# Performance work log

Measured on AMD Instinct MI355X. Metric: run time of the kernel, lower is better.

Reference implementation:

```python
import jax, jax.numpy as jnp
import numpy as np

LN2 = jnp.log(jnp.float32(2.0))
ALPHA = 0.5          # alpha_pool = [0.5]
A_BITS = 8           # activation bit width (BIT_TYPE_A)
W_BITS = 8           # weight bit width (BIT_TYPE_W)
EPS = 1e-8


def round_ln(x):
    # 'round' branch: floor(log2(x)) then pick nearer power of two
    y = jnp.floor(jnp.log(x) / LN2)
    up = (x - 2.0 ** y) > (2.0 ** (y + 1.0) - x)
    return y + up.astype(x.dtype)


def fq_act_asym(x, bits=A_BITS):
    # per-tensor asymmetric uniform fake-quant (QAct min-max observer)
    qmax = 2 ** bits - 1
    xmin = jnp.minimum(x.min(), 0.0)
    xmax = jnp.maximum(x.max(), 0.0)
    scale = jnp.maximum((xmax - xmin) / qmax, EPS)
    zp = jnp.round(-xmin / scale)
    q = jnp.clip(jnp.round(x / scale) + zp, 0, qmax)
    return (q - zp) * scale


def fq_act_sym(x, bits=A_BITS):
    # per-tensor symmetric fake-quant (qact1 with asymmetric=False)
    qmax = 2 ** (bits - 1) - 1
    scale = jnp.maximum(jnp.abs(x).max() / qmax, EPS)
    q = jnp.clip(jnp.round(x / scale), -qmax - 1, qmax)
    return q * scale


def fq_weight(w, bits=W_BITS):
    # per-output-channel symmetric weight fake-quant (QLinear)
    qmax = 2 ** (bits - 1) - 1
    scale = jnp.maximum(jnp.abs(w).max(axis=1, keepdims=True) / qmax, EPS)
    q = jnp.clip(jnp.round(w / scale), -qmax - 1, qmax)
    return q * scale


def setup_inputs() -> dict:
    key = jax.random.key(0)
    ks = jax.random.split(key, 5)
    B, N, C, H = 64, 197, 768, 3072
    x = jax.random.normal(ks[0], (B, N, C), dtype=jnp.float32)
    w1 = jax.random.normal(ks[1], (H, C), dtype=jnp.float32) * 0.02
    b1 = jax.random.normal(ks[2], (H,), dtype=jnp.float32) * 0.02
    w2 = jax.random.normal(ks[3], (C, H), dtype=jnp.float32) * 0.02
    b2 = jax.random.normal(ks[4], (C,), dtype=jnp.float32) * 0.02
    return {"x": x, "w1": w1, "b1": b1, "w2": w2, "b2": b2}


def reference(x, w1, b1, w2, b2):
    # ---- smoothquant power-of-two channel scale (fc1 input channels) ----
    global_max_x = jnp.abs(x).max(axis=(0, 1))      # [C]
    max_weight = jnp.abs(w1).max(axis=0)            # [C]
    cs = global_max_x ** ALPHA / max_weight ** (1.0 - ALPHA)
    cs = 2.0 ** round_ln(cs)                        # snap to power of two
    x_smoothed = x / cs[None, None, :]
    w1_smoothed = w1 * cs[None, :]
    # ---- qact0 -> fc1 (8-bit fake-quant GEMM) ----
    xq = fq_act_asym(x_smoothed)
    h = jnp.einsum('bnc,hc->bnh', xq, fq_weight(w1_smoothed)) + b1
    # ---- act (exact GELU, nn.GELU default) -> qact1 (symmetric) ----
    h = jax.nn.gelu(h, approximate=False)
    hq = fq_act_sym(h)
    # ---- fc2 -> qact2 ----
    out = jnp.einsum('bnh,ch->bnc', hq, fq_weight(w2)) + b2
    out = fq_act_asym(out)
    return out
```

## Files before the change

### kernel.cpp

```cpp
#include <hip/hip_runtime.h>
#include <cstdint>
#include <cstddef>

typedef int v4i __attribute__((ext_vector_type(4)));

#define DI static __device__ __forceinline__

DI unsigned fmap(float f){ unsigned b=__float_as_uint(f); return (b&0x80000000u)? ~b : (b|0x80000000u); }
DI float funmap(unsigned u){ return (u&0x80000000u)? __uint_as_float(u&0x7fffffffu) : __uint_as_float(~u); }
DI float gelu_f(float x){ return 0.5f*x*(1.0f+erff(x*0.70710678118654752440f)); }

constexpr int Mtok = 12608;
constexpr int Cdim = 768;
constexpr int Hdim = 3072;
constexpr int MP   = 12672;

__global__ void k_init(unsigned* scal, unsigned* xminU, unsigned* xmaxU, unsigned* wmaxU){
    int t = blockIdx.x*256 + threadIdx.x;
    if (t < Cdim){
        xminU[t] = fmap(__builtin_inff());
        xmaxU[t] = fmap(-__builtin_inff());
        wmaxU[t] = fmap(0.0f);
    }
    if (t == 0){
        scal[0] = fmap(0.0f);
        scal[1] = fmap(__builtin_inff());
        scal[2] = fmap(-__builtin_inff());
    }
}

__global__ void k_colstats_x(const float* __restrict__ x, unsigned* xminU, unsigned* xmaxU){
    int t = threadIdx.x;
    float mn0= __builtin_inff(), mn1= __builtin_inff(), mn2= __builtin_inff();
    float mx0=-__builtin_inff(), mx1=-__builtin_inff(), mx2=-__builtin_inff();
    for (int r = blockIdx.x; r < Mtok; r += gridDim.x){
        const float* row = x + (size_t)r*Cdim;
        float v0=row[t], v1=row[t+256], v2=row[t+512];
        mn0=fminf(mn0,v0); mx0=fmaxf(mx0,v0);
        mn1=fminf(mn1,v1); mx1=fmaxf(mx1,v1);
        mn2=fminf(mn2,v2); mx2=fmaxf(mx2,v2);
    }
    atomicMin(&xminU[t      ], fmap(mn0)); atomicMax(&xmaxU[t      ], fmap(mx0));
    atomicMin(&xminU[t+256  ], fmap(mn1)); atomicMax(&xmaxU[t+256  ], fmap(mx1));
    atomicMin(&xminU[t+512  ], fmap(mn2)); atomicMax(&xmaxU[t+512  ], fmap(mx2));
}

__global__ void k_colmax_w1(const float* __restrict__ w1, unsigned* wmaxU){
    int t = threadIdx.x;
    float m0=0.f, m1=0.f, m2=0.f;
    for (int r = blockIdx.x; r < Hdim; r += gridDim.x){
        const float* row = w1 + (size_t)r*Cdim;
        m0=fmaxf(m0,fabsf(row[t]));
        m1=fmaxf(m1,fabsf(row[t+256]));
        m2=fmaxf(m2,fabsf(row[t+512]));
    }
    atomicMax(&wmaxU[t      ], fmap(m0));
    atomicMax(&wmaxU[t+256  ], fmap(m1));
    atomicMax(&wmaxU[t+512  ], fmap(m2));
}

__global__ void k_scale0(const unsigned* xminU, const unsigned* xmaxU, const unsigned* wmaxU,
                         float* cs, unsigned* scal){
    __shared__ float smn[256], smx[256];
    int t = threadIdx.x;
    float lmn =  __builtin_inff(), lmx = -__builtin_inff();
    #pragma unroll
    for (int j = 0; j < 3; ++j){
        int c = t + j*256;
        float xn = funmap(xminU[c]), xm = funmap(xmaxU[c]), wm = funmap(wmaxU[c]);
        float g  = fmaxf(fabsf(xn), fabsf(xm));
        float csr = powf(g, 0.5f) / powf(wm, 0.5f);
        float y = floorf(logf(csr) / 0.6931471805599453f);
        float p = exp2f(y);
        float c2 = exp2f(y + (((csr - p) > (2.0f*p - csr)) ? 1.0f : 0.0f));
        cs[c] = c2;
        lmn = fminf(lmn, xn / c2);
        lmx = fmaxf(lmx, xm / c2);
    }
    smn[t]=lmn; smx[t]=lmx; __syncthreads();
    for (int s=128; s; s>>=1){
        if (t < s){ smn[t]=fminf(smn[t],smn[t+s]); smx[t]=fmaxf(smx[t],smx[t+s]); }
        __syncthreads();
    }
    if (t == 0){
        float xmin_t = fminf(smn[0], 0.0f);
        float xmax_t = fmaxf(smx[0], 0.0f);
        float sc = fmaxf((xmax_t - xmin_t)/255.0f, 1e-8f);
        float zp = rintf(-xmin_t/sc);
        float* fs = (float*)scal;
        fs[8] = sc; fs[9] = zp;
    }
}

__global__ void k_quant_w1(const float* __restrict__ w1, const float* __restrict__ cs,
                           const unsigned* scal, int8_t* __restrict__ qw1,
                           float* sa1, int* icorr1){
    __shared__ float sm[256];
    __shared__ int   si[256];
    int h = blockIdx.x, t = threadIdx.x;
    const float* wr = w1 + (size_t)h*Cdim;
    float v0 = wr[t]*cs[t], v1 = wr[t+256]*cs[t+256], v2 = wr[t+512]*cs[t+512];
    float am = fmaxf(fabsf(v0), fmaxf(fabsf(v1), fabsf(v2)));
    sm[t]=am; __syncthreads();
    for (int s=128; s; s>>=1){ if (t<s) sm[t]=fmaxf(sm[t],sm[t+s]); __syncthreads(); }
    float scale = fmaxf(sm[0]/127.0f, 1e-8f);
    float q0 = fminf(fmaxf(rintf(v0/scale), -128.0f), 127.0f);
    float q1 = fminf(fmaxf(rintf(v1/scale), -128.0f), 127.0f);
    float q2 = fminf(fmaxf(rintf(v2/scale), -128.0f), 127.0f);
    qw1[(size_t)h*Cdim + t      ] = (int8_t)q0;
    qw1[(size_t)h*Cdim + t + 256] = (int8_t)q1;
    qw1[(size_t)h*Cdim + t + 512] = (int8_t)q2;
    si[t] = (int)q0 + (int)q1 + (int)q2; __syncthreads();
    for (int s=128; s; s>>=1){ if (t<s) si[t]+=si[t+s]; __syncthreads(); }
    if (t == 0){
        const float* fs = (const float*)scal;
        sa1[h]    = fs[8]*scale;
        icorr1[h] = (128 - (int)fs[9]) * si[0];
    }
}

__global__ void k_quant_w2(const float* __restrict__ w2, int8_t* __restrict__ qw2, float* sa2){
    __shared__ float sm[256];
    int c = blockIdx.x, t = threadIdx.x;
    const float* wr = w2 + (size_t)c*Hdim;
    float v[12]; float am = 0.f;
    #pragma unroll
    for (int j=0;j<12;++j){ v[j]=wr[t + j*256]; am=fmaxf(am,fabsf(v[j])); }
    sm[t]=am; __syncthreads();
    for (int s=128; s; s>>=1){ if (t<s) sm[t]=fmaxf(sm[t],sm[t+s]); __syncthreads(); }
    float scale = fmaxf(sm[0]/127.0f, 1e-8f);
    #pragma unroll
    for (int j=0;j<12;++j){
        float q = fminf(fmaxf(rintf(v[j]/scale), -128.0f), 127.0f);
        qw2[(size_t)c*Hdim + t + j*256] = (int8_t)q;
    }
    if (t == 0) sa2[c] = scale;
}

__global__ void k_quant_x(const float* __restrict__ x, const float* __restrict__ cs,
                          const unsigned* scal, int8_t* __restrict__ qxs){
    int idx = blockIdx.x*256 + threadIdx.x;
    const int total = Mtok*(Cdim/4);
    if (idx >= total) return;
    const float* fs = (const float*)scal;
    float sc = fs[8], zp = fs[9];
    float4 v = ((const float4*)x)[idx];
    int cb = (idx % (Cdim/4))*4;
    float q0 = fminf(fmaxf(rintf((v.x/cs[cb+0])/sc)+zp, 0.f), 255.f);
    float q1 = fminf(fmaxf(rintf((v.y/cs[cb+1])/sc)+zp, 0.f), 255.f);
    float q2 = fminf(fmaxf(rintf((v.z/cs[cb+2])/sc)+zp, 0.f), 255.f);
    float q3 = fminf(fmaxf(rintf((v.w/cs[cb+3])/sc)+zp, 0.f), 255.f);
    uint32_t pack =  (uint32_t)(uint8_t)((int)q0-128)
                  | ((uint32_t)(uint8_t)((int)q1-128) << 8)
                  | ((uint32_t)(uint8_t)((int)q2-128) << 16)
                  | ((uint32_t)(uint8_t)((int)q3-128) << 24);
    ((uint32_t*)qxs)[idx] = pack;
}

#define GLL(src,dst) __builtin_amdgcn_global_load_lds( \
    (const __attribute__((address_space(1))) unsigned*)(src), \
    (__attribute__((address_space(3))) unsigned*)(dst), 16, 0, 0)

#define WAITVM8 asm volatile("s_waitcnt vmcnt(8)" ::: "memory")
#define WAITVM4 asm volatile("s_waitcnt vmcnt(4)" ::: "memory")
#define WAITVM0 asm volatile("s_waitcnt vmcnt(0)" ::: "memory")

template<int KSTEPS, int MODE, int NY>
__global__ __launch_bounds__(256)
void k_gemm(const int8_t* __restrict__ A, const int8_t* __restrict__ Bw, int N,
            const float* __restrict__ sa, const int* __restrict__ icorr,
            const float* __restrict__ bias, const unsigned* __restrict__ scal,
            int8_t* __restrict__ qout, float* __restrict__ fout, _Float16* __restrict__ hout,
            unsigned* __restrict__ r0, unsigned* __restrict__ r1)
{
    constexpr int K = KSTEPS*64;
    __shared__ __align__(16) int8_t LDSB[49152];
    __shared__ float sred[8];
    int t = threadIdx.x, lane = t & 63, wid = t >> 6;
    int wr = wid >> 1, wc = wid & 1;

    int nwg = gridDim.x;
    int q8 = nwg >> 3, r8 = nwg & 7;
    int xcd = blockIdx.x & 7, li = blockIdx.x >> 3;
    int swz = (xcd < r8 ? xcd*(q8+1) : r8*(q8+1) + (xcd - r8)*q8) + li;
    int bx = swz / NY, by = swz % NY;
    size_t brow = (size_t)bx * 128;
    int bcol = by * 128;

    int srow = t >> 2;
    int schunk = (t & 3) ^ ((srow >> 1) & 3);
    const int8_t* ga0 = A  + (brow + srow)*(size_t)K + schunk*16;
    const int8_t* gb0 = Bw + (size_t)(bcol + srow)*K + schunk*16;

    int rsw  = ((lane >> 4) ^ ((lane >> 1) & 3)) << 4;
    int aoff = ((wr*64 + (lane & 15)) << 6) + rsw;
    int boff = 8192 + ((wc*64 + (lane & 15)) << 6) + rsw;

    float sav[4], bbv[4]; int icv[4]; float sh = 0.f;
    #pragma unroll
    for (int n=0;n<4;++n){
        int col = bcol + wc*64 + n*16 + (lane & 15);
        sav[n] = sa[col];
        bbv[n] = bias[col];
        icv[n] = (MODE == 2) ? 0 : icorr[col];
    }
    if (MODE == 1 || MODE == 2) sh = fmaxf(funmap(*scal)/127.0f, 1e-8f);
    asm volatile("" ::: "memory");

#define STAGE(cur, ks) do{ \
    const int8_t* pa_ = ga0 + (ks)*64; \
    const int8_t* pb_ = gb0 + (ks)*64; \
    int8_t* ld_ = LDSB + (cur)*16384 + t*16; \
    GLL(pa_,                ld_); \
    GLL(pa_ + (size_t)64*K, ld_ + 4096); \
    GLL(pb_,                ld_ + 8192); \
    GLL(pb_ + (size_t)64*K, ld_ + 12288); \
}while(0)

    v4i acc[4][4] = {};
    STAGE(0,0); STAGE(1,1); STAGE(2,2);

#define ITER(cur, ks, WAITM, RESTAGE) do{ \
    WAITM;                                    \
    __builtin_amdgcn_s_barrier();             \
    const int8_t* bp_ = LDSB + (cur)*16384; \
    v4i a_[4], b_[4]; \
    _Pragma("unroll") \
    for (int m_=0;m_<4;++m_) a_[m_] = *(const v4i*)(bp_ + aoff + (m_<<10)); \
    _Pragma("unroll") \
    for (int n_=0;n_<4;++n_) b_[n_] = *(const v4i*)(bp_ + boff + (n_<<10)); \
    asm volatile("s_waitcnt lgkmcnt(0)" ::: "memory"); \
    __builtin_amdgcn_sched_barrier(0); \
    __builtin_amdgcn_s_barrier();             \
    if (RESTAGE) STAGE(cur, (ks)+3); \
    __builtin_amdgcn_s_setprio(1); \
    _Pragma("unroll") \
    for (int m_=0;m_<4;++m_) \
        _Pragma("unroll") \
        for (int n_=0;n_<4;++n_) \
            acc[m_][n_] = __builtin_amdgcn_mfma_i32_16x16x64_i8(a_[m_], b_[n_], acc[m_][n_], 0, 0, 0); \
    __builtin_amdgcn_s_setprio(0); \
}while(0)

    constexpr int MAING = (KSTEPS - 3)/3;
    for (int kg = 0; kg < MAING; ++kg){
        int ks = kg*3;
        ITER(0, ks,   WAITVM8, true);
        ITER(1, ks+1, WAITVM8, true);
        ITER(2, ks+2, WAITVM8, true);
    }
    ITER(0, KSTEPS-3, WAITVM8, false);
    ITER(1, KSTEPS-2, WAITVM4, false);
    ITER(2, KSTEPS-1, WAITVM0, false);
#undef ITER
#undef STAGE

    int rl = (lane >> 4) * 4;
    if (MODE == 0){
        float amax = 0.f;
        #pragma unroll
        for (int n=0;n<4;++n){
            #pragma unroll
            for (int m=0;m<4;++m){
                size_t row = brow + wr*64 + m*16 + rl;
                #pragma unroll
                for (int r=0;r<4;++r){
                    if (row + r < (size_t)Mtok){
                        float g = gelu_f(sav[n]*(float)(acc[m][n][r] + icv[n]) + bbv[n]);
                        amax = fmaxf(amax, fabsf(g));
                    }
                }
            }
        }
        #pragma unroll
        for (int off=32; off; off>>=1) amax = fmaxf(amax, __shfl_down(amax, off));
        if (lane == 0) sred[wid] = amax;
        __syncthreads();
        if (t == 0) atomicMax(r0, fmap(fmaxf(fmaxf(sred[0],sred[1]), fmaxf(sred[2],sred[3]))));
    } else if (MODE == 1){
        #pragma unroll
        for (int n=0;n<4;++n){
            int col = bcol + wc*64 + n*16 + (lane & 15);
            #pragma unroll
            for (int m=0;m<4;++m){
                size_t row = brow + wr*64 + m*16 + rl;
                #pragma unroll
                for (int r=0;r<4;++r){
                    if (row + r < (size_t)Mtok){
                        float g = gelu_f(sav[n]*(float)(acc[m][n][r] + icv[n]) + bbv[n]);
                        float qv = fminf(fmaxf(rintf(g/sh), -128.0f), 127.0f);
                        qout[(row + r)*(size_t)N + col] = (int8_t)qv;
                    }
                }
            }
        }
    } else if (MODE == 3){
        float amax = 0.f;
        _Float16* hb = hout + ((size_t)(bx*NY + by))*16384 + (size_t)t*64;
        #pragma unroll
        for (int n=0;n<4;++n){
            #pragma unroll
            for (int m=0;m<4;++m){
                size_t row = brow + wr*64 + m*16 + rl;
                union { _Float16 h4[4]; uint2 u2; } pk;
                #pragma unroll
                for (int r=0;r<4;++r){
                    float g = gelu_f(sav[n]*(float)(acc[m][n][r] + icv[n]) + bbv[n]);
                    if (row + r < (size_t)Mtok) amax = fmaxf(amax, fabsf(g));
                    pk.h4[r] = (_Float16)g;
                }
                ((uint2*)hb)[n*4 + m] = pk.u2;
            }
        }
        #pragma unroll
        for (int off=32; off; off>>=1) amax = fmaxf(amax, __shfl_down(amax, off));
        if (lane == 0) sred[wid] = amax;
        __syncthreads();
        if (t == 0) atomicMax(r0, fmap(fmaxf(fmaxf(sred[0],sred[1]), fmaxf(sred[2],sred[3]))));
    } else {
        float lmin =  __builtin_inff(), lmax = -__builtin_inff();
        float* ob = fout + ((size_t)(bx*NY + by))*16384 + (size_t)t*64;
        #pragma unroll
        for (int n=0;n<4;++n){
            float s = sh * sav[n];
            #pragma unroll
            for (int m=0;m<4;++m){
                size_t row = brow + wr*64 + m*16 + rl;
                float4 o4;
                #pragma unroll
                for (int r=0;r<4;++r){
                    float o = s*(float)acc[m][n][r] + bbv[n];
                    if (row + r < (size_t)Mtok){ lmin = fminf(lmin, o); lmax = fmaxf(lmax, o); }
                    ((float*)&o4)[r] = o;
                }
                ((float4*)ob)[n*4 + m] = o4;
            }
        }
        #pragma unroll
        for (int off=32; off; off>>=1){
            lmin = fminf(lmin, __shfl_down(lmin, off));
            lmax = fmaxf(lmax, __shfl_down(lmax, off));
        }
        if (lane == 0){ sred[wid] = lmin; sred[4+wid] = lmax; }
        __syncthreads();
        if (t == 0){
            atomicMin(r0, fmap(fminf(fminf(sred[0],sred[1]), fminf(sred[2],sred[3]))));
            atomicMax(r1, fmap(fmaxf(fmaxf(sred[4],sred[5]), fmaxf(sred[6],sred[7]))));
        }
    }
}

__global__ void k_requant(const _Float16* __restrict__ h, const unsigned* __restrict__ scal,
                          int8_t* __restrict__ qh){
    int idx = blockIdx.x*256 + threadIdx.x;
    const int total = Mtok*(Hdim/8);
    if (idx >= total) return;
    float sh = fmaxf(funmap(scal[0])/127.0f, 1e-8f);
    int R  = idx / 384;
    int cb = (idx - R*384) * 8;
    int bx = R >> 7, r0 = R & 127;
    int by = cb >> 7;
    int wr = r0 >> 6, m = (r0 >> 4) & 3, lhi = (r0 >> 2) & 3, r = r0 & 3;
    int wc = (cb >> 6) & 1, n = (cb >> 4) & 3, li0 = cb & 15;
    int tb = (wr*2 + wc)*64 + lhi*16 + li0;
    const _Float16* p = h + ((size_t)(bx*24 + by))*16384 + (size_t)tb*64 + ((n*4 + m)*4 + r);
    uint32_t lo = 0, hi = 0;
    #pragma unroll
    for (int j=0;j<4;++j){
        float q = fminf(fmaxf(rintf((float)p[j*64]/sh), -128.0f), 127.0f);
        lo |= ((uint32_t)(uint8_t)(int)q) << (8*j);
    }
    #pragma unroll
    for (int j=0;j<4;++j){
        float q = fminf(fmaxf(rintf((float)p[(4+j)*64]/sh), -128.0f), 127.0f);
        hi |= ((uint32_t)(uint8_t)(int)q) << (8*j);
    }
    uint2 pk; pk.x = lo; pk.y = hi;
    ((uint2*)qh)[idx] = pk;
}

__global__ void k_final(const float* __restrict__ outpre, const unsigned* __restrict__ scal,
                        float* __restrict__ out){
    int idx = blockIdx.x*256 + threadIdx.x;
    const int total = Mtok*(Cdim/4);
    if (idx >= total) return;
    float omin = fminf(funmap(scal[1]), 0.0f);
    float omax = fmaxf(funmap(scal[2]), 0.0f);
    float sc = fmaxf((omax - omin)/255.0f, 1e-8f);
    float zp = rintf(-omin/sc);
    int R  = idx / 192;
    int cb = (idx - R*192) * 4;
    int bx = R >> 7, r0 = R & 127;
    int by = cb >> 7;
    int wr = r0 >> 6, m = (r0 >> 4) & 3, lhi = (r0 >> 2) & 3, r = r0 & 3;
    int wc = (cb >> 6) & 1, n = (cb >> 4) & 3, li0 = cb & 15;
    int tb = (wr*2 + wc)*64 + lhi*16 + li0;
    const float* p = outpre + ((size_t)(bx*6 + by))*16384 + (size_t)tb*64 + ((n*4 + m)*4 + r);
    float4 v;
    v.x = p[0]; v.y = p[64]; v.z = p[128]; v.w = p[192];
    v.x = (fminf(fmaxf(rintf(v.x/sc)+zp, 0.f), 255.f) - zp)*sc;
    v.y = (fminf(fmaxf(rintf(v.y/sc)+zp, 0.f), 255.f) - zp)*sc;
    v.z = (fminf(fmaxf(rintf(v.z/sc)+zp, 0.f), 255.f) - zp)*sc;
    v.w = (fminf(fmaxf(rintf(v.w/sc)+zp, 0.f), 255.f) - zp)*sc;
    ((float4*)out)[idx] = v;
}

extern "C" void kernel_launch(void* const* d_in, const int* in_sizes, int n_in,
                              void* d_out, int out_size, void* d_ws, size_t ws_size,
                              hipStream_t stream)
{
    if (n_in < 5) return;
    const float* x  = (const float*)d_in[0];
    const float* w1 = (const float*)d_in[1];
    const float* b1 = (const float*)d_in[2];
    const float* w2 = (const float*)d_in[3];
    const float* b2 = (const float*)d_in[4];
    float* out = (float*)d_out;

    uint8_t* w = (uint8_t*)d_ws;
    size_t off = 0;
    unsigned* scal  = (unsigned*)(w + off); off += 256;
    unsigned* xminU = (unsigned*)(w + off); off += 3072;
    unsigned* xmaxU = (unsigned*)(w + off); off += 3072;
    unsigned* wmaxU = (unsigned*)(w + off); off += 3072;
    float*    cs    = (float*)   (w + off); off += 3072;
    float*    sa1   = (float*)   (w + off); off += 12288;
    int*      icorr1= (int*)     (w + off); off += 12288;
    float*    sa2   = (float*)   (w + off); off += 3072;
    off = (off + 255) & ~(size_t)255;
    int8_t*   qw1   = (int8_t*)  (w + off); off += (size_t)Hdim*Cdim;
    int8_t*   qw2   = (int8_t*)  (w + off); off += (size_t)Cdim*Hdim;
    int8_t*   qxs   = (int8_t*)  (w + off); off += (size_t)MP*Cdim;
    int8_t*   qh    = (int8_t*)  (w + off); off += (size_t)MP*Hdim;
    size_t off_big = off;
    float*    outpre= (float*)   (w + off_big);
    _Float16* hbuf  = (_Float16*)(w + off_big);
    size_t need_3g  = off_big + (size_t)99*6*16384*4;
    size_t need_h16 = off_big + (size_t)99*24*16384*2;
    if (ws_size < need_3g) return;
    bool use_h16 = (ws_size >= need_h16);

    k_init<<<3, 256, 0, stream>>>(scal, xminU, xmaxU, wmaxU);
    k_colstats_x<<<512, 256, 0, stream>>>(x, xminU, xmaxU);
    k_colmax_w1<<<512, 256, 0, stream>>>(w1, wmaxU);
    k_scale0<<<1, 256, 0, stream>>>(xminU, xmaxU, wmaxU, cs, scal);
    k_quant_w1<<<Hdim, 256, 0, stream>>>(w1, cs, scal, qw1, sa1, icorr1);
    k_quant_w2<<<Cdim, 256, 0, stream>>>(w2, qw2, sa2);
    k_quant_x<<<(Mtok*(Cdim/4) + 255)/256, 256, 0, stream>>>(x, cs, scal, qxs);

    if (use_h16){
        k_gemm<12,3,24><<<2376, 256, 0, stream>>>(qxs, qw1, Hdim, sa1, icorr1, b1, scal,
                                                  nullptr, nullptr, hbuf, &scal[0], nullptr);
        k_requant<<<(Mtok*(Hdim/8) + 255)/256, 256, 0, stream>>>(hbuf, scal, qh);
    } else {
        k_gemm<12,0,24><<<2376, 256, 0, stream>>>(qxs, qw1, Hdim, sa1, icorr1, b1, scal,
                                                  nullptr, nullptr, nullptr, &scal[0], nullptr);
        k_gemm<12,1,24><<<2376, 256, 0, stream>>>(qxs, qw1, Hdim, sa1, icorr1, b1, scal,
                                                  qh, nullptr, nullptr, nullptr, nullptr);
    }
    k_gemm<48,2,6><<<594, 256, 0, stream>>>(qh, qw2, Cdim, sa2, nullptr, b2, scal,
                                            nullptr, outpre, nullptr, &scal[1], &scal[2]);

    k_final<<<(Mtok*(Cdim/4) + 255)/256, 256, 0, stream>>>(outpre, scal, out);
}
```

Baseline: 387.5 us.

## Load GEMM B operand directly to registers and coalesce staged epilogue writes

```diff
diff --git a/kernel.cpp b/kernel.cpp
--- a/kernel.cpp
+++ b/kernel.cpp
@@ -161,10 +161,6 @@
     (const __attribute__((address_space(1))) unsigned*)(src), \
     (__attribute__((address_space(3))) unsigned*)(dst), 16, 0, 0)
 
-#define WAITVM8 asm volatile("s_waitcnt vmcnt(8)" ::: "memory")
-#define WAITVM4 asm volatile("s_waitcnt vmcnt(4)" ::: "memory")
-#define WAITVM0 asm volatile("s_waitcnt vmcnt(0)" ::: "memory")
-
 template<int KSTEPS, int MODE, int NY>
 __global__ __launch_bounds__(256)
 void k_gemm(const int8_t* __restrict__ A, const int8_t* __restrict__ Bw, int N,
@@ -174,7 +170,7 @@
             unsigned* __restrict__ r0, unsigned* __restrict__ r1)
 {
     constexpr int K = KSTEPS*64;
-    __shared__ __align__(16) int8_t LDSB[49152];
+    __shared__ __align__(16) int8_t LDSB[24576];
     __shared__ float sred[8];
     int t = threadIdx.x, lane = t & 63, wid = t >> 6;
     int wr = wid >> 1, wc = wid & 1;
@@ -190,11 +186,11 @@
     int srow = t >> 2;
     int schunk = (t & 3) ^ ((srow >> 1) & 3);
     const int8_t* ga0 = A  + (brow + srow)*(size_t)K + schunk*16;
-    const int8_t* gb0 = Bw + (size_t)(bcol + srow)*K + schunk*16;
+
+    const int8_t* gB = Bw + (size_t)(bcol + wc*64 + (lane & 15))*K + ((lane >> 4) << 4);
 
     int rsw  = ((lane >> 4) ^ ((lane >> 1) & 3)) << 4;
     int aoff = ((wr*64 + (lane & 15)) << 6) + rsw;
-    int boff = 8192 + ((wc*64 + (lane & 15)) << 6) + rsw;
 
     float sav[4], bbv[4]; int icv[4]; float sh = 0.f;
     #pragma unroll
@@ -207,51 +203,62 @@
     if (MODE == 1 || MODE == 2) sh = fmaxf(funmap(*scal)/127.0f, 1e-8f);
     asm volatile("" ::: "memory");
 
-#define STAGE(cur, ks) do{ \
+#define STAGE(sb, ks) do{ \
     const int8_t* pa_ = ga0 + (ks)*64; \
-    const int8_t* pb_ = gb0 + (ks)*64; \
-    int8_t* ld_ = LDSB + (cur)*16384 + t*16; \
+    int8_t* ld_ = LDSB + (sb)*8192 + t*16; \
     GLL(pa_,                ld_); \
     GLL(pa_ + (size_t)64*K, ld_ + 4096); \
-    GLL(pb_,                ld_ + 8192); \
-    GLL(pb_ + (size_t)64*K, ld_ + 12288); \
 }while(0)
 
     v4i acc[4][4] = {};
-    STAGE(0,0); STAGE(1,1); STAGE(2,2);
-
-#define ITER(cur, ks, WAITM, RESTAGE) do{ \
-    WAITM;                                    \
-    __builtin_amdgcn_s_barrier();             \
-    const int8_t* bp_ = LDSB + (cur)*16384; \
-    v4i a_[4], b_[4]; \
+    v4i bcur[4];
+
+    STAGE(0,0);
+    __builtin_amdgcn_sched_barrier(0);
+    #pragma unroll
+    for (int n=0;n<4;++n) bcur[n] = *(const v4i*)(gB + (size_t)n*(16*K));
+    __builtin_amdgcn_sched_barrier(0);
+    STAGE(1,1);
+
+#define ITER(cur, ks, WAITN, HASB, HASSTAGE) do{ \
+    asm volatile("s_waitcnt vmcnt(" #WAITN ")" ::: "memory"); \
+    __builtin_amdgcn_s_barrier(); \
+    v4i bn_[4]; \
+    if (HASB){ \
+        _Pragma("unroll") \
+        for (int n_=0;n_<4;++n_) bn_[n_] = *(const v4i*)(gB + (size_t)n_*(16*K) + ((ks)+1)*64); \
+    } \
+    __builtin_amdgcn_sched_barrier(0); \
+    if (HASSTAGE) STAGE(((cur)+2)%3, (ks)+2); \
+    const int8_t* bp_ = LDSB + (cur)*8192; \
+    v4i a_[4]; \
     _Pragma("unroll") \
     for (int m_=0;m_<4;++m_) a_[m_] = *(const v4i*)(bp_ + aoff + (m_<<10)); \
-    _Pragma("unroll") \
-    for (int n_=0;n_<4;++n_) b_[n_] = *(const v4i*)(bp_ + boff + (n_<<10)); \
     asm volatile("s_waitcnt lgkmcnt(0)" ::: "memory"); \
     __builtin_amdgcn_sched_barrier(0); \
-    __builtin_amdgcn_s_barrier();             \
-    if (RESTAGE) STAGE(cur, (ks)+3); \
     __builtin_amdgcn_s_setprio(1); \
     _Pragma("unroll") \
     for (int m_=0;m_<4;++m_) \
         _Pragma("unroll") \
         for (int n_=0;n_<4;++n_) \
-            acc[m_][n_] = __builtin_amdgcn_mfma_i32_16x16x64_i8(a_[m_], b_[n_], acc[m_][n_], 0, 0, 0); \
+            acc[m_][n_] = __builtin_amdgcn_mfma_i32_16x16x64_i8(a_[m_], bcur[n_], acc[m_][n_], 0, 0, 0); \
     __builtin_amdgcn_s_setprio(0); \
+    if (HASB){ \
+        _Pragma("unroll") \
+        for (int n_=0;n_<4;++n_) bcur[n_] = bn_[n_]; \
+    } \
 }while(0)
 
-    constexpr int MAING = (KSTEPS - 3)/3;
+    constexpr int MAING = KSTEPS/3 - 1;
     for (int kg = 0; kg < MAING; ++kg){
         int ks = kg*3;
-        ITER(0, ks,   WAITVM8, true);
-        ITER(1, ks+1, WAITVM8, true);
-        ITER(2, ks+2, WAITVM8, true);
-    }
-    ITER(0, KSTEPS-3, WAITVM8, false);
-    ITER(1, KSTEPS-2, WAITVM4, false);
-    ITER(2, KSTEPS-1, WAITVM0, false);
+        ITER(0, ks,   2, true, true);
+        ITER(1, ks+1, 2, true, true);
+        ITER(2, ks+2, 2, true, true);
+    }
+    ITER(0, KSTEPS-3, 2, true,  true);
+    ITER(1, KSTEPS-2, 2, true,  false);
+    ITER(2, KSTEPS-1, 0, false, false);
 #undef ITER
 #undef STAGE
 
@@ -296,7 +303,7 @@
         }
     } else if (MODE == 3){
         float amax = 0.f;
-        _Float16* hb = hout + ((size_t)(bx*NY + by))*16384 + (size_t)t*64;
+        _Float16* hb = hout + ((size_t)(bx*NY + by))*16384 + wid*4096 + lane*4;
         #pragma unroll
         for (int n=0;n<4;++n){
             #pragma unroll
@@ -309,7 +316,7 @@
                     if (row + r < (size_t)Mtok) amax = fmaxf(amax, fabsf(g));
                     pk.h4[r] = (_Float16)g;
                 }
-                ((uint2*)hb)[n*4 + m] = pk.u2;
+                *(uint2*)(hb + (n*4+m)*256) = pk.u2;
             }
         }
         #pragma unroll
@@ -319,7 +326,7 @@
         if (t == 0) atomicMax(r0, fmap(fmaxf(fmaxf(sred[0],sred[1]), fmaxf(sred[2],sred[3]))));
     } else {
         float lmin =  __builtin_inff(), lmax = -__builtin_inff();
-        float* ob = fout + ((size_t)(bx*NY + by))*16384 + (size_t)t*64;
+        float* ob = fout + ((size_t)(bx*NY + by))*16384 + wid*4096 + lane*4;
         #pragma unroll
         for (int n=0;n<4;++n){
             float s = sh * sav[n];
@@ -333,7 +340,7 @@
                     if (row + r < (size_t)Mtok){ lmin = fminf(lmin, o); lmax = fmaxf(lmax, o); }
                     ((float*)&o4)[r] = o;
                 }
-                ((float4*)ob)[n*4 + m] = o4;
+                *(float4*)(ob + (n*4+m)*256) = o4;
             }
         }
         #pragma unroll
@@ -359,20 +366,21 @@
     int R  = idx / 384;
     int cb = (idx - R*384) * 8;
     int bx = R >> 7, r0 = R & 127;
-    int by = cb >> 7;
-    int wr = r0 >> 6, m = (r0 >> 4) & 3, lhi = (r0 >> 2) & 3, r = r0 & 3;
-    int wc = (cb >> 6) & 1, n = (cb >> 4) & 3, li0 = cb & 15;
-    int tb = (wr*2 + wc)*64 + lhi*16 + li0;
-    const _Float16* p = h + ((size_t)(bx*24 + by))*16384 + (size_t)tb*64 + ((n*4 + m)*4 + r);
+    int by = cb >> 7, c0 = cb & 127;
+    int wid2 = (r0 >> 6)*2 + (c0 >> 6);
+    int m = (r0 >> 4) & 3, n = (c0 >> 4) & 3;
+    int lane2 = ((r0 >> 2) & 3)*16 + (c0 & 15);
+    int r = r0 & 3;
+    const _Float16* p = h + ((size_t)(bx*24 + by))*16384 + wid2*4096 + (n*4+m)*256 + lane2*4 + r;
     uint32_t lo = 0, hi = 0;
     #pragma unroll
     for (int j=0;j<4;++j){
-        float q = fminf(fmaxf(rintf((float)p[j*64]/sh), -128.0f), 127.0f);
+        float q = fminf(fmaxf(rintf((float)p[4*j]/sh), -128.0f), 127.0f);
         lo |= ((uint32_t)(uint8_t)(int)q) << (8*j);
     }
     #pragma unroll
     for (int j=0;j<4;++j){
-        float q = fminf(fmaxf(rintf((float)p[(4+j)*64]/sh), -128.0f), 127.0f);
+        float q = fminf(fmaxf(rintf((float)p[4*(4+j)]/sh), -128.0f), 127.0f);
         hi |= ((uint32_t)(uint8_t)(int)q) << (8*j);
     }
     uint2 pk; pk.x = lo; pk.y = hi;
@@ -391,13 +399,14 @@
     int R  = idx / 192;
     int cb = (idx - R*192) * 4;
     int bx = R >> 7, r0 = R & 127;
-    int by = cb >> 7;
-    int wr = r0 >> 6, m = (r0 >> 4) & 3, lhi = (r0 >> 2) & 3, r = r0 & 3;
-    int wc = (cb >> 6) & 1, n = (cb >> 4) & 3, li0 = cb & 15;
-    int tb = (wr*2 + wc)*64 + lhi*16 + li0;
-    const float* p = outpre + ((size_t)(bx*6 + by))*16384 + (size_t)tb*64 + ((n*4 + m)*4 + r);
+    int by = cb >> 7, c0 = cb & 127;
+    int wid2 = (r0 >> 6)*2 + (c0 >> 6);
+    int m = (r0 >> 4) & 3, n = (c0 >> 4) & 3;
+    int lane2 = ((r0 >> 2) & 3)*16 + (c0 & 15);
+    int r = r0 & 3;
+    const float* p = outpre + ((size_t)(bx*6 + by))*16384 + wid2*4096 + (n*4+m)*256 + lane2*4 + r;
     float4 v;
-    v.x = p[0]; v.y = p[64]; v.z = p[128]; v.w = p[192];
+    v.x = p[0]; v.y = p[4]; v.z = p[8]; v.w = p[12];
     v.x = (fminf(fmaxf(rintf(v.x/sc)+zp, 0.f), 255.f) - zp)*sc;
     v.y = (fminf(fmaxf(rintf(v.y/sc)+zp, 0.f), 255.f) - zp)*sc;
     v.z = (fminf(fmaxf(rintf(v.z/sc)+zp, 0.f), 255.f) - zp)*sc;
```

Measured after the change: 442.5 us. 14.2% more time.
